# Kernel optimization log

Measured on AMD Instinct MI355X. Metric: run time of the kernel, lower is better.

The kernel has to match this reference:

```python
import jax, jax.numpy as jnp
import numpy as np

B, P = 4, 2048
NUM_MODS, D_TIME = 22, 8
DIM_S = NUM_MODS + D_TIME + 1          # 31
PHI_W, PSI_W, PSI_LAT = 32, 32, 32
DOT, HEADS, RHO_W = 16, 4, 64


def _xavier(key, shape):
    fan_in, fan_out = shape[0], shape[1]
    std = (2.0 / (fan_in + fan_out)) ** 0.5
    return jax.random.normal(key, shape, jnp.float32) * std


def setup_inputs() -> dict:
    key = jax.random.key(0)
    ks = jax.random.split(key, 20)
    inp = {
        "times": jnp.sort(jax.random.uniform(ks[0], (B, P), jnp.float32) * 100.0, axis=1),
        "values": jax.random.normal(ks[1], (B, P), jnp.float32),
        "measurements": jax.random.randint(ks[2], (B, P), 0, NUM_MODS + 1, jnp.int64 if jax.config.jax_enable_x64 else jnp.int32),
        "non_pad_mask": jnp.ones((B, P, 1), jnp.float32),
        # attention.psi MLP_state(dim_s -> psi_width)
        "psi_w1": _xavier(ks[3], (DIM_S, PSI_W)), "psi_b1": jnp.zeros((PSI_W,), jnp.float32),
        "psi_w2": _xavier(ks[4], (PSI_W, PSI_W)), "psi_b2": jnp.zeros((PSI_W,), jnp.float32),
        # attention.rho Linear(psi_width -> psi_latent_width)
        "arho_w": _xavier(ks[5], (PSI_W, PSI_LAT)), "arho_b": jnp.zeros((PSI_LAT,), jnp.float32),
        # attention key/query projections
        "W_k": _xavier(ks[6], (PSI_LAT + DIM_S, DOT * HEADS)),
        "W_q": _xavier(ks[7], (HEADS, DOT)),
        # phi MLP_state(dim_s -> phi_width)
        "phi_w1": _xavier(ks[8], (DIM_S, PHI_W)), "phi_b1": jnp.zeros((PHI_W,), jnp.float32),
        "phi_w2": _xavier(ks[9], (PHI_W, PHI_W)), "phi_b2": jnp.zeros((PHI_W,), jnp.float32),
        # rho MLP_state(n_heads*phi_width -> rho_width)
        "rho_w1": _xavier(ks[10], (HEADS * PHI_W, RHO_W)), "rho_b1": jnp.zeros((RHO_W,), jnp.float32),
        "rho_w2": _xavier(ks[11], (RHO_W, RHO_W)), "rho_b2": jnp.zeros((RHO_W,), jnp.float32),
    }
    return inp


def _mlp_state(x, mask, w1, b1, w2, b2):
    # MLP_state: relu(fc1(x*mask)); relu(fc2(h*mask)); h*mask  (dropout p=0)
    h = jax.nn.relu((x * mask) @ w1 + b1)
    h = jax.nn.relu((h * mask) @ w2 + b2)
    return h * mask


def _forward(times, values, measurements, non_pad_mask,
             psi_w1, psi_b1, psi_w2, psi_b2, arho_w, arho_b, W_k, W_q,
             phi_w1, phi_b1, phi_w2, phi_b2, rho_w1, rho_b1, rho_w2, rho_b2):
    mask = non_pad_mask  # [B,P,1]
    # temporal encoding: time / 10000^(2*(i//2)/d_time), sin on even, cos on odd
    idx = jnp.arange(D_TIME)
    pos_vec = jnp.power(10000.0, 2.0 * (idx // 2).astype(jnp.float32) / D_TIME)
    r = times[:, :, None] / pos_vec[None, None, :]          # [B,P,d_time]
    tenc = jnp.where(idx % 2 == 0, jnp.sin(r), jnp.cos(r))
    # one-hot measurements, drop padding channel 0
    meas = jax.nn.one_hot(measurements, NUM_MODS + 1, dtype=jnp.float32)[:, :, 1:]
    combined = jnp.concatenate([tenc, values[:, :, None], meas], axis=-1)  # [B,P,dim_s]

    # --- CumulativeSetAttentionLayer ---
    enc_psi = _mlp_state(combined, mask, psi_w1, psi_b1, psi_w2, psi_b2)   # [B,P,psi_w]
    counts = jnp.arange(1, P + 1, dtype=jnp.float32)[None, :, None]
    agg = jnp.cumsum(enc_psi, axis=1) / counts * mask                      # cumulative mean
    agg = (agg @ arho_w + arho_b) * mask                                   # [B,P,psi_lat]
    comb2 = jnp.concatenate([combined, agg], axis=-1)                      # [B,P,dim_s+psi_lat]
    keys = (comb2 @ W_k) * mask                                            # [B,P,DOT*HEADS]
    # torch.split(keys, n_heads, -1) + stack(-1): chunk i has size HEADS -> [B,P,HEADS,DOT]
    keys = keys.reshape(B, P, DOT, HEADS).transpose(0, 1, 3, 2)            # [B,P,h,d]
    preattn = jnp.einsum('bphd,hd->bph', keys, W_q) / jnp.sqrt(jnp.float32(DOT))
    preattn = preattn * mask                                               # [B,P,m]

    # --- phi encoding ---
    enc = _mlp_state(combined, mask, phi_w1, phi_b1, phi_w2, phi_b2)       # [B,P,d_phi]

    # --- cumulative causal softmax weighting ---
    A = preattn[:, None, :, :]                                             # [B,1,Q,m]
    Bc = jax.lax.cummax(preattn, axis=1)[:, :, None, :]                    # [B,P,1,m]
    triu = jnp.triu(jnp.ones((P, P), bool), 1)[None, :, :, None]           # mask Q > P
    D = jnp.exp(jnp.where(triu, -jnp.inf, A - Bc))                          # [B,P,Q,m]
    E = jnp.sum(D, axis=2)                                                 # [B,P,m]
    out5 = jnp.einsum('bpqm,bqd->bpmd', D, enc) / E[:, :, :, None]
    out5 = out5 * mask[:, :, :, None]                                      # [B,P,m,d_phi]

    agg2 = out5.reshape(B, P, HEADS * PHI_W)
    output = _mlp_state(agg2, mask, rho_w1, rho_b1, rho_w2, rho_b2)        # [B,P,rho_w]
    return output


def reference(times, values, measurements, non_pad_mask,
              psi_w1, psi_b1, psi_w2, psi_b2, arho_w, arho_b, W_k, W_q,
              phi_w1, phi_b1, phi_w2, phi_b2, rho_w1, rho_b1, rho_w2, rho_b2):
    return _forward(times, values, measurements, non_pad_mask,
                    psi_w1, psi_b1, psi_w2, psi_b2, arho_w, arho_b, W_k, W_q,
                    phi_w1, phi_b1, phi_w2, phi_b2, rho_w1, rho_b1, rho_w2, rho_b2)
```

## Files before the change

kernel.cpp:

```cpp
#include <hip/hip_runtime.h>
#include <math.h>

#define PB 2048
#define OFF_ENC 0
#define OFF_Q   262144
#define OFF_R   294912
#define OFF_MSK 327680
#define OFF_WV  335872

__global__ __launch_bounds__(64) void k_encode(
    const float* __restrict__ times, const float* __restrict__ vals,
    const int* __restrict__ meas, const float* __restrict__ mask,
    const float* __restrict__ psi_w1, const float* __restrict__ psi_b1,
    const float* __restrict__ psi_w2, const float* __restrict__ psi_b2,
    const float* __restrict__ phi_w1, const float* __restrict__ phi_b1,
    const float* __restrict__ phi_w2, const float* __restrict__ phi_b2,
    const float* __restrict__ arho_w, const float* __restrict__ arho_b,
    const float* __restrict__ W_k, const float* __restrict__ W_q,
    float* __restrict__ ws)
{
    __shared__ float sW[4222];
    __shared__ float sU[31*4];
    __shared__ float sU2[32*4];
    __shared__ float sV[32*4];
    __shared__ float sCc[4];
    for (int i = threadIdx.x; i < 1023; i += 64) {
        int r = i / 33, cc = i - r * 33;
        sW[i]        = (cc < 32) ? psi_w1[r*32 + cc] : 0.0f;
        sW[2111 + i] = (cc < 32) ? phi_w1[r*32 + cc] : 0.0f;
    }
    for (int i = threadIdx.x; i < 1024; i += 64) {
        sW[1055 + i] = psi_w2[i];
        sW[3166 + i] = phi_w2[i];
    }
    if (threadIdx.x < 32) {
        int i = threadIdx.x;
        sW[1023 + i] = psi_b1[i];
        sW[2079 + i] = psi_b2[i];
        sW[3134 + i] = phi_b1[i];
        sW[4190 + i] = phi_b2[i];
    }
    for (int t = threadIdx.x; t < 252; t += 64) {
        int i = t >> 2, h = t & 3;
        float s = 0.0f;
        #pragma unroll
        for (int d = 0; d < 16; d++)
            s = fmaf(W_k[i*64 + d*4 + h], W_q[h*16 + d], s);
        s *= 0.25f;
        if (i < 31) sU[i*4 + h] = s; else sU2[(i-31)*4 + h] = s;
    }
    __syncthreads();
    for (int t = threadIdx.x; t < 128; t += 64) {
        int ch = t >> 2, h = t & 3;
        float s = 0.0f;
        #pragma unroll
        for (int j = 0; j < 32; j++)
            s = fmaf(arho_w[ch*32 + j], sU2[j*4 + h], s);
        sV[t] = s;
    }
    if (threadIdx.x < 4) {
        float s = 0.0f;
        #pragma unroll
        for (int j = 0; j < 32; j++)
            s = fmaf(arho_b[j], sU2[j*4 + threadIdx.x], s);
        sCc[threadIdx.x] = s;
    }
    __syncthreads();

    const int tid  = threadIdx.x;
    const int qd   = tid >> 4;
    const int jb   = qd << 3;
    const int pp = blockIdx.x * 16 + (tid & 15);
    const int b = pp >> 11, p = pp & 2047;
    const float t = times[pp];
    const float v = vals[pp];
    const float msk = mask[pp];
    const int m = meas[pp];

    float c[9];
    c[0] = sinf(t);           c[1] = cosf(t);
    c[2] = sinf(t * 0.1f);    c[3] = cosf(t * 0.1f);
    c[4] = sinf(t * 0.01f);   c[5] = cosf(t * 0.01f);
    c[6] = sinf(t * 0.001f);  c[7] = cosf(t * 0.001f);
    c[8] = v;

    float* enc_t = ws + OFF_ENC;
    const int cb = b * 32;

    float x[9];
    #pragma unroll
    for (int i = 0; i < 9; i++) x[i] = c[i] * msk;
    const float ohs = (m > 0) ? msk : 0.0f;
    const int   ohr = (m > 0) ? (8 + m) * 33 : 0;

    if (qd == 0) {
        float r[4] = {sCc[0], sCc[1], sCc[2], sCc[3]};
        #pragma unroll
        for (int i = 0; i < 9; i++) {
            #pragma unroll
            for (int h = 0; h < 4; h++) r[h] = fmaf(c[i], sU[i*4 + h], r[h]);
        }
        if (m > 0) {
            #pragma unroll
            for (int h = 0; h < 4; h++) r[h] += sU[(8 + m)*4 + h];
        }
        #pragma unroll
        for (int h = 0; h < 4; h++)
            ws[OFF_R + (size_t)(b*4 + h) * PB + p] = r[h];
        ws[OFF_MSK + (size_t)b * PB + p] = msk;
    }

    const bool hi1 = (qd & 1) != 0;
    const bool hi2 = (qd >> 1) != 0;

    {
        float h1o[8];
        #pragma unroll
        for (int jj = 0; jj < 8; jj++) {
            const int j = jb + jj;
            float acc = sW[1023 + j];
            #pragma unroll
            for (int i = 0; i < 9; i++) acc = fmaf(x[i], sW[i*33 + j], acc);
            acc = fmaf(ohs, sW[ohr + j], acc);
            h1o[jj] = fmaxf(acc, 0.0f) * msk;
        }
        float hA[16];
        #pragma unroll
        for (int jj = 0; jj < 8; jj++) {
            const float other = __shfl_xor(h1o[jj], 16);
            hA[jj]     = hi1 ? other   : h1o[jj];
            hA[8 + jj] = hi1 ? h1o[jj] : other;
        }
        float h1f[32];
        #pragma unroll
        for (int jj = 0; jj < 16; jj++) {
            const float other = __shfl_xor(hA[jj], 32);
            h1f[jj]      = hi2 ? other  : hA[jj];
            h1f[16 + jj] = hi2 ? hA[jj] : other;
        }
        float q[4] = {0.f, 0.f, 0.f, 0.f};
        #pragma unroll
        for (int jj = 0; jj < 8; jj++) {
            const int j = jb + jj;
            float acc = sW[2079 + j];
            #pragma unroll
            for (int i = 0; i < 32; i++) acc = fmaf(h1f[i], sW[1055 + i*32 + j], acc);
            const float p2 = fmaxf(acc, 0.0f) * msk;
            #pragma unroll
            for (int h = 0; h < 4; h++) q[h] = fmaf(p2, sV[j*4 + h], q[h]);
        }
        #pragma unroll
        for (int h = 0; h < 4; h++) {
            q[h] += __shfl_xor(q[h], 16);
            q[h] += __shfl_xor(q[h], 32);
        }
        if (qd == 0) {
            #pragma unroll
            for (int h = 0; h < 4; h++)
                ws[OFF_Q + (size_t)(b*4 + h) * PB + p] = q[h];
        }
    }
    {
        float h1o[8];
        #pragma unroll
        for (int jj = 0; jj < 8; jj++) {
            const int j = jb + jj;
            float acc = sW[3134 + j];
            #pragma unroll
            for (int i = 0; i < 9; i++) acc = fmaf(x[i], sW[2111 + i*33 + j], acc);
            acc = fmaf(ohs, sW[2111 + ohr + j], acc);
            h1o[jj] = fmaxf(acc, 0.0f) * msk;
        }
        float hA[16];
        #pragma unroll
        for (int jj = 0; jj < 8; jj++) {
            const float other = __shfl_xor(h1o[jj], 16);
            hA[jj]     = hi1 ? other   : h1o[jj];
            hA[8 + jj] = hi1 ? h1o[jj] : other;
        }
        float h1f[32];
        #pragma unroll
        for (int jj = 0; jj < 16; jj++) {
            const float other = __shfl_xor(hA[jj], 32);
            h1f[jj]      = hi2 ? other  : hA[jj];
            h1f[16 + jj] = hi2 ? hA[jj] : other;
        }
        #pragma unroll
        for (int jj = 0; jj < 8; jj++) {
            const int j = jb + jj;
            float acc = sW[4190 + j];
            #pragma unroll
            for (int i = 0; i < 32; i++) acc = fmaf(h1f[i], sW[3166 + i*32 + j], acc);
            enc_t[(size_t)(cb + j) * PB + p] = fmaxf(acc, 0.0f) * msk;
        }
    }
}

__global__ __launch_bounds__(64) void k_mid(float* __restrict__ ws)
{
    const int blk = blockIdx.x;
    const int bh = blk / 33;
    const int c  = blk - bh * 33;
    const int b  = bh >> 2;
    const int lane = threadIdx.x;

    const float4* q4 = (const float4*)(ws + OFF_Q   + (size_t)bh * PB + lane * 32);
    const float4* r4 = (const float4*)(ws + OFF_R   + (size_t)bh * PB + lane * 32);
    const float4* m4 = (const float4*)(ws + OFF_MSK + (size_t)b  * PB + lane * 32);
    const float4* e4 = (const float4*)(ws + OFF_ENC + ((size_t)(b*32 + (c-1))) * PB + lane * 32);
    float4* o4 = (float4*)(ws + OFF_WV + ((size_t)(bh*33 + c)) * PB + lane * 32);

    float vq[32];
    #pragma unroll
    for (int k = 0; k < 8; k++) {
        float4 f = q4[k];
        vq[4*k] = f.x; vq[4*k+1] = f.y; vq[4*k+2] = f.z; vq[4*k+3] = f.w;
    }
    #pragma unroll
    for (int j = 1; j < 32; j++) vq[j] += vq[j-1];
    {
        const float tot = vq[31];
        float x = tot;
        #pragma unroll
        for (int off = 1; off < 64; off <<= 1) {
            float y = __shfl_up(x, off);
            if (lane >= off) x += y;
        }
        const float excl = x - tot;
        #pragma unroll
        for (int j = 0; j < 32; j++) vq[j] += excl;
    }
    float v[32];
    #pragma unroll
    for (int k = 0; k < 8; k++) {
        const float4 fr = r4[k];
        const float4 fm = m4[k];
        const int p0 = lane * 32 + 4*k;
        v[4*k+0] = expf(fm.x * (fr.x + vq[4*k+0] / (float)(p0 + 1)));
        v[4*k+1] = expf(fm.y * (fr.y + vq[4*k+1] / (float)(p0 + 2)));
        v[4*k+2] = expf(fm.z * (fr.z + vq[4*k+2] / (float)(p0 + 3)));
        v[4*k+3] = expf(fm.w * (fr.w + vq[4*k+3] / (float)(p0 + 4)));
    }
    if (c > 0) {
        #pragma unroll
        for (int k = 0; k < 8; k++) {
            float4 f = e4[k];
            v[4*k] *= f.x; v[4*k+1] *= f.y; v[4*k+2] *= f.z; v[4*k+3] *= f.w;
        }
    }
    #pragma unroll
    for (int j = 1; j < 32; j++) v[j] += v[j-1];
    const float tot = v[31];
    float x = tot;
    #pragma unroll
    for (int off = 1; off < 64; off <<= 1) {
        float y = __shfl_up(x, off);
        if (lane >= off) x += y;
    }
    const float excl = x - tot;
    #pragma unroll
    for (int j = 0; j < 32; j++) v[j] += excl;
    #pragma unroll
    for (int k = 0; k < 8; k++)
        o4[k] = make_float4(v[4*k], v[4*k+1], v[4*k+2], v[4*k+3]);
}

__global__ __launch_bounds__(256) void k_rho(
    const float* __restrict__ rho_w1, const float* __restrict__ rho_b1,
    const float* __restrict__ rho_w2, const float* __restrict__ rho_b2,
    const float* __restrict__ ws, float* __restrict__ out)
{
    __shared__ float h1s[16][65];
    __shared__ float scl[16][4];
    __shared__ float mskS[16];
    const int tid = threadIdx.x;
    const int pos = tid >> 4;
    const int g   = tid & 15;
    const int pbase = blockIdx.x * 16;
    const int b  = pbase >> 11;
    const int p0 = pbase & 2047;
    const float* wv = ws + OFF_WV + (size_t)b * 132 * PB;

    if (tid < 64) {
        const int pp = tid >> 2, h = tid & 3;
        const float msk = ws[OFF_MSK + (size_t)b * PB + p0 + pp];
        const float L = wv[(size_t)(h*33) * PB + p0 + pp];
        scl[pp][h] = msk / L;
        if (h == 0) mskS[pp] = msk;
    }
    __syncthreads();

    const int pg = p0 + pos;
    float4 acc = ((const float4*)rho_b1)[g];
    const float4* w14 = (const float4*)rho_w1;
    const float sc0 = scl[pos][0], sc1 = scl[pos][1];
    const float sc2 = scl[pos][2], sc3 = scl[pos][3];
    #pragma unroll
    for (int h = 0; h < 4; h++) {
        const float sc = (h == 0) ? sc0 : (h == 1) ? sc1 : (h == 2) ? sc2 : sc3;
        const float* wvh = wv + (size_t)(h*33 + 1) * PB + pg;
        #pragma unroll 8
        for (int d = 0; d < 32; d++) {
            const float ai = wvh[(size_t)d * PB] * sc;
            const float4 w = w14[(h*32 + d)*16 + g];
            acc.x = fmaf(ai, w.x, acc.x);
            acc.y = fmaf(ai, w.y, acc.y);
            acc.z = fmaf(ai, w.z, acc.z);
            acc.w = fmaf(ai, w.w, acc.w);
        }
    }
    const float msk = mskS[pos];
    h1s[pos][g*4+0] = fmaxf(acc.x, 0.f) * msk;
    h1s[pos][g*4+1] = fmaxf(acc.y, 0.f) * msk;
    h1s[pos][g*4+2] = fmaxf(acc.z, 0.f) * msk;
    h1s[pos][g*4+3] = fmaxf(acc.w, 0.f) * msk;
    __syncthreads();

    float4 acc2 = ((const float4*)rho_b2)[g];
    const float4* w24 = (const float4*)rho_w2;
    #pragma unroll 16
    for (int i = 0; i < 64; i++) {
        const float hv = h1s[pos][i];
        const float4 w = w24[i*16 + g];
        acc2.x = fmaf(hv, w.x, acc2.x);
        acc2.y = fmaf(hv, w.y, acc2.y);
        acc2.z = fmaf(hv, w.z, acc2.z);
        acc2.w = fmaf(hv, w.w, acc2.w);
    }
    float4 o;
    o.x = fmaxf(acc2.x, 0.f) * msk;
    o.y = fmaxf(acc2.y, 0.f) * msk;
    o.z = fmaxf(acc2.z, 0.f) * msk;
    o.w = fmaxf(acc2.w, 0.f) * msk;
    ((float4*)out)[(size_t)(pbase + pos) * 16 + g] = o;
}

extern "C" void kernel_launch(void* const* d_in, const int* in_sizes, int n_in,
                              void* d_out, int out_size, void* d_ws, size_t ws_size,
                              hipStream_t stream)
{
    const float* times  = (const float*)d_in[0];
    const float* vals   = (const float*)d_in[1];
    const int*   meas   = (const int*)d_in[2];
    const float* mask   = (const float*)d_in[3];
    const float* psi_w1 = (const float*)d_in[4];
    const float* psi_b1 = (const float*)d_in[5];
    const float* psi_w2 = (const float*)d_in[6];
    const float* psi_b2 = (const float*)d_in[7];
    const float* arho_w = (const float*)d_in[8];
    const float* arho_b = (const float*)d_in[9];
    const float* W_k    = (const float*)d_in[10];
    const float* W_q    = (const float*)d_in[11];
    const float* phi_w1 = (const float*)d_in[12];
    const float* phi_b1 = (const float*)d_in[13];
    const float* phi_w2 = (const float*)d_in[14];
    const float* phi_b2 = (const float*)d_in[15];
    const float* rho_w1 = (const float*)d_in[16];
    const float* rho_b1 = (const float*)d_in[17];
    const float* rho_w2 = (const float*)d_in[18];
    const float* rho_b2 = (const float*)d_in[19];
    float* ws  = (float*)d_ws;
    float* out = (float*)d_out;

    k_encode<<<dim3(512), dim3(64), 0, stream>>>(times, vals, meas, mask,
        psi_w1, psi_b1, psi_w2, psi_b2, phi_w1, phi_b1, phi_w2, phi_b2,
        arho_w, arho_b, W_k, W_q, ws);
    k_mid<<<dim3(528), dim3(64), 0, stream>>>(ws);
    k_rho<<<dim3(512), dim3(256), 0, stream>>>(rho_w1, rho_b1, rho_w2, rho_b2, ws, out);
}
```

Measured before the change: 132.6 us.

## Split encode MLP output columns across 8 lanes with float4 LDS weight reads

```diff
diff --git a/kernel.cpp b/kernel.cpp
--- a/kernel.cpp
+++ b/kernel.cpp
@@ -8,7 +8,17 @@
 #define OFF_MSK 327680
 #define OFF_WV  335872
 
-__global__ __launch_bounds__(64) void k_encode(
+#define S_PSI_W1 0
+#define S_PSI_B1 1116
+#define S_PSI_W2 1148
+#define S_PSI_B2 2172
+#define S_PHI_W1 2204
+#define S_PHI_B1 3320
+#define S_PHI_W2 3352
+#define S_PHI_B2 4376
+#define S_TOT    4408
+
+__global__ __launch_bounds__(128) void k_encode(
     const float* __restrict__ times, const float* __restrict__ vals,
     const int* __restrict__ meas, const float* __restrict__ mask,
     const float* __restrict__ psi_w1, const float* __restrict__ psi_b1,
@@ -19,58 +29,84 @@
     const float* __restrict__ W_k, const float* __restrict__ W_q,
     float* __restrict__ ws)
 {
-    __shared__ float sW[4222];
-    __shared__ float sU[31*4];
-    __shared__ float sU2[32*4];
-    __shared__ float sV[32*4];
-    __shared__ float sCc[4];
-    for (int i = threadIdx.x; i < 1023; i += 64) {
-        int r = i / 33, cc = i - r * 33;
-        sW[i]        = (cc < 32) ? psi_w1[r*32 + cc] : 0.0f;
-        sW[2111 + i] = (cc < 32) ? phi_w1[r*32 + cc] : 0.0f;
-    }
-    for (int i = threadIdx.x; i < 1024; i += 64) {
-        sW[1055 + i] = psi_w2[i];
-        sW[3166 + i] = phi_w2[i];
-    }
-    if (threadIdx.x < 32) {
-        int i = threadIdx.x;
-        sW[1023 + i] = psi_b1[i];
-        sW[2079 + i] = psi_b2[i];
-        sW[3134 + i] = phi_b1[i];
-        sW[4190 + i] = phi_b2[i];
-    }
-    for (int t = threadIdx.x; t < 252; t += 64) {
-        int i = t >> 2, h = t & 3;
-        float s = 0.0f;
-        #pragma unroll
-        for (int d = 0; d < 16; d++)
-            s = fmaf(W_k[i*64 + d*4 + h], W_q[h*16 + d], s);
-        s *= 0.25f;
-        if (i < 31) sU[i*4 + h] = s; else sU2[(i-31)*4 + h] = s;
+    __shared__ __align__(16) float sW[S_TOT];
+    __shared__ __align__(16) float sU[31*4];
+    __shared__ __align__(16) float sU2[32*4];
+    __shared__ __align__(16) float sV[32*4];
+    __shared__ __align__(16) float sCc[4];
+
+    const int tid = threadIdx.x;
+
+    {
+        const float4* a4 = (const float4*)psi_w1;
+        const float4* b4 = (const float4*)phi_w1;
+        float4* d1 = (float4*)&sW[S_PSI_W1];
+        float4* d2 = (float4*)&sW[S_PHI_W1];
+        for (int i = tid; i < 248; i += 128) {
+            const int r = i >> 3, c4 = i & 7;
+            d1[r*9 + c4] = a4[i];
+            d2[r*9 + c4] = b4[i];
+        }
+    }
+    {
+        const float4* p4 = (const float4*)psi_w2;
+        const float4* f4 = (const float4*)phi_w2;
+        float4* s1 = (float4*)&sW[S_PSI_W2];
+        float4* s2 = (float4*)&sW[S_PHI_W2];
+        for (int i = tid; i < 256; i += 128) { s1[i] = p4[i]; s2[i] = f4[i]; }
+    }
+    if (tid < 32) {
+        sW[S_PSI_B1 + tid] = psi_b1[tid];
+        sW[S_PSI_B2 + tid] = psi_b2[tid];
+        sW[S_PHI_B1 + tid] = phi_b1[tid];
+        sW[S_PHI_B2 + tid] = phi_b2[tid];
+    }
+    if (tid < 63) {
+        const int i = tid;
+        const float4* wk4 = (const float4*)(W_k + i*64);
+        float4 s = make_float4(0.f, 0.f, 0.f, 0.f);
+        #pragma unroll
+        for (int d = 0; d < 16; d++) {
+            const float4 w = wk4[d];
+            s.x = fmaf(w.x, W_q[d],      s.x);
+            s.y = fmaf(w.y, W_q[16 + d], s.y);
+            s.z = fmaf(w.z, W_q[32 + d], s.z);
+            s.w = fmaf(w.w, W_q[48 + d], s.w);
+        }
+        s.x *= 0.25f; s.y *= 0.25f; s.z *= 0.25f; s.w *= 0.25f;
+        if (i < 31) *(float4*)&sU[i*4]        = s;
+        else        *(float4*)&sU2[(i-31)*4]  = s;
     }
     __syncthreads();
-    for (int t = threadIdx.x; t < 128; t += 64) {
-        int ch = t >> 2, h = t & 3;
-        float s = 0.0f;
-        #pragma unroll
-        for (int j = 0; j < 32; j++)
-            s = fmaf(arho_w[ch*32 + j], sU2[j*4 + h], s);
-        sV[t] = s;
-    }
-    if (threadIdx.x < 4) {
-        float s = 0.0f;
-        #pragma unroll
-        for (int j = 0; j < 32; j++)
-            s = fmaf(arho_b[j], sU2[j*4 + threadIdx.x], s);
-        sCc[threadIdx.x] = s;
+    if (tid < 32) {
+        const float* aw = arho_w + tid*32;
+        float4 s = make_float4(0.f, 0.f, 0.f, 0.f);
+        #pragma unroll
+        for (int j = 0; j < 32; j++) {
+            const float a = aw[j];
+            const float4 u = *(const float4*)&sU2[j*4];
+            s.x = fmaf(a, u.x, s.x); s.y = fmaf(a, u.y, s.y);
+            s.z = fmaf(a, u.z, s.z); s.w = fmaf(a, u.w, s.w);
+        }
+        *(float4*)&sV[tid*4] = s;
+    } else if (tid == 32) {
+        float4 s = make_float4(0.f, 0.f, 0.f, 0.f);
+        #pragma unroll
+        for (int j = 0; j < 32; j++) {
+            const float a = arho_b[j];
+            const float4 u = *(const float4*)&sU2[j*4];
+            s.x = fmaf(a, u.x, s.x); s.y = fmaf(a, u.y, s.y);
+            s.z = fmaf(a, u.z, s.z); s.w = fmaf(a, u.w, s.w);
+        }
+        *(float4*)&sCc[0] = s;
     }
     __syncthreads();
 
-    const int tid  = threadIdx.x;
-    const int qd   = tid >> 4;
-    const int jb   = qd << 3;
-    const int pp = blockIdx.x * 16 + (tid & 15);
+    const int wv_  = tid >> 6;
+    const int lane = tid & 63;
+    const int qd   = lane >> 3;
+    const int jb   = qd << 2;
+    const int pp = blockIdx.x * 16 + wv_ * 8 + (lane & 7);
     const int b = pp >> 11, p = pp & 2047;
     const float t = times[pp];
     const float v = vals[pp];
@@ -91,66 +127,94 @@
     #pragma unroll
     for (int i = 0; i < 9; i++) x[i] = c[i] * msk;
     const float ohs = (m > 0) ? msk : 0.0f;
-    const int   ohr = (m > 0) ? (8 + m) * 33 : 0;
+    const int   ohr = (m > 0) ? (8 + m) * 36 : 0;
 
     if (qd == 0) {
-        float r[4] = {sCc[0], sCc[1], sCc[2], sCc[3]};
+        float4 r = *(const float4*)&sCc[0];
         #pragma unroll
         for (int i = 0; i < 9; i++) {
-            #pragma unroll
-            for (int h = 0; h < 4; h++) r[h] = fmaf(c[i], sU[i*4 + h], r[h]);
+            const float4 u = *(const float4*)&sU[i*4];
+            const float cv = c[i];
+            r.x = fmaf(cv, u.x, r.x); r.y = fmaf(cv, u.y, r.y);
+            r.z = fmaf(cv, u.z, r.z); r.w = fmaf(cv, u.w, r.w);
         }
         if (m > 0) {
-            #pragma unroll
-            for (int h = 0; h < 4; h++) r[h] += sU[(8 + m)*4 + h];
-        }
-        #pragma unroll
-        for (int h = 0; h < 4; h++)
-            ws[OFF_R + (size_t)(b*4 + h) * PB + p] = r[h];
+            const float4 u = *(const float4*)&sU[(8 + m)*4];
+            r.x += u.x; r.y += u.y; r.z += u.z; r.w += u.w;
+        }
+        ws[OFF_R + (size_t)(b*4 + 0) * PB + p] = r.x;
+        ws[OFF_R + (size_t)(b*4 + 1) * PB + p] = r.y;
+        ws[OFF_R + (size_t)(b*4 + 2) * PB + p] = r.z;
+        ws[OFF_R + (size_t)(b*4 + 3) * PB + p] = r.w;
         ws[OFF_MSK + (size_t)b * PB + p] = msk;
     }
 
-    const bool hi1 = (qd & 1) != 0;
-    const bool hi2 = (qd >> 1) != 0;
+    const bool hiA = (qd & 1) != 0;
+    const bool hiB = (qd & 2) != 0;
+    const bool hiC = (qd & 4) != 0;
 
     {
-        float h1o[8];
+        float4 a1 = *(const float4*)&sW[S_PSI_B1 + jb];
+        #pragma unroll
+        for (int i = 0; i < 9; i++) {
+            const float4 w = *(const float4*)&sW[S_PSI_W1 + i*36 + jb];
+            const float xv = x[i];
+            a1.x = fmaf(xv, w.x, a1.x); a1.y = fmaf(xv, w.y, a1.y);
+            a1.z = fmaf(xv, w.z, a1.z); a1.w = fmaf(xv, w.w, a1.w);
+        }
+        {
+            const float4 w = *(const float4*)&sW[S_PSI_W1 + ohr + jb];
+            a1.x = fmaf(ohs, w.x, a1.x); a1.y = fmaf(ohs, w.y, a1.y);
+            a1.z = fmaf(ohs, w.z, a1.z); a1.w = fmaf(ohs, w.w, a1.w);
+        }
+        float h1o[4];
+        h1o[0] = fmaxf(a1.x, 0.f) * msk; h1o[1] = fmaxf(a1.y, 0.f) * msk;
+        h1o[2] = fmaxf(a1.z, 0.f) * msk; h1o[3] = fmaxf(a1.w, 0.f) * msk;
+
+        float hA[8];
+        #pragma unroll
+        for (int jj = 0; jj < 4; jj++) {
+            const float other = __shfl_xor(h1o[jj], 8);
+            hA[jj]     = hiA ? other   : h1o[jj];
+            hA[4 + jj] = hiA ? h1o[jj] : other;
+        }
+        float hB[16];
         #pragma unroll
         for (int jj = 0; jj < 8; jj++) {
-            const int j = jb + jj;
-            float acc = sW[1023 + j];
-            #pragma unroll
-            for (int i = 0; i < 9; i++) acc = fmaf(x[i], sW[i*33 + j], acc);
-            acc = fmaf(ohs, sW[ohr + j], acc);
-            h1o[jj] = fmaxf(acc, 0.0f) * msk;
-        }
-        float hA[16];
-        #pragma unroll
-        for (int jj = 0; jj < 8; jj++) {
-            const float other = __shfl_xor(h1o[jj], 16);
-            hA[jj]     = hi1 ? other   : h1o[jj];
-            hA[8 + jj] = hi1 ? h1o[jj] : other;
+            const float other = __shfl_xor(hA[jj], 16);
+            hB[jj]     = hiB ? other  : hA[jj];
+            hB[8 + jj] = hiB ? hA[jj] : other;
         }
         float h1f[32];
         #pragma unroll
         for (int jj = 0; jj < 16; jj++) {
-            const float other = __shfl_xor(hA[jj], 32);
-            h1f[jj]      = hi2 ? other  : hA[jj];
-            h1f[16 + jj] = hi2 ? hA[jj] : other;
-        }
+            const float other = __shfl_xor(hB[jj], 32);
+            h1f[jj]      = hiC ? other  : hB[jj];
+            h1f[16 + jj] = hiC ? hB[jj] : other;
+        }
+        float4 a2 = *(const float4*)&sW[S_PSI_B2 + jb];
+        #pragma unroll
+        for (int i = 0; i < 32; i++) {
+            const float4 w = *(const float4*)&sW[S_PSI_W2 + i*32 + jb];
+            const float hv = h1f[i];
+            a2.x = fmaf(hv, w.x, a2.x); a2.y = fmaf(hv, w.y, a2.y);
+            a2.z = fmaf(hv, w.z, a2.z); a2.w = fmaf(hv, w.w, a2.w);
+        }
+        float p2[4];
+        p2[0] = fmaxf(a2.x, 0.f) * msk; p2[1] = fmaxf(a2.y, 0.f) * msk;
+        p2[2] = fmaxf(a2.z, 0.f) * msk; p2[3] = fmaxf(a2.w, 0.f) * msk;
         float q[4] = {0.f, 0.f, 0.f, 0.f};
         #pragma unroll
-        for (int jj = 0; jj < 8; jj++) {
-            const int j = jb + jj;
-            float acc = sW[2079 + j];
-            #pragma unroll
-            for (int i = 0; i < 32; i++) acc = fmaf(h1f[i], sW[1055 + i*32 + j], acc);
-            const float p2 = fmaxf(acc, 0.0f) * msk;
-            #pragma unroll
-            for (int h = 0; h < 4; h++) q[h] = fmaf(p2, sV[j*4 + h], q[h]);
+        for (int jj = 0; jj < 4; jj++) {
+            const float4 vv = *(const float4*)&sV[(jb + jj)*4];
+            q[0] = fmaf(p2[jj], vv.x, q[0]);
+            q[1] = fmaf(p2[jj], vv.y, q[1]);
+            q[2] = fmaf(p2[jj], vv.z, q[2]);
+            q[3] = fmaf(p2[jj], vv.w, q[3]);
         }
         #pragma unroll
         for (int h = 0; h < 4; h++) {
+            q[h] += __shfl_xor(q[h], 8);
             q[h] += __shfl_xor(q[h], 16);
             q[h] += __shfl_xor(q[h], 32);
         }
@@ -161,38 +225,56 @@
         }
     }
     {
-        float h1o[8];
+        float4 a1 = *(const float4*)&sW[S_PHI_B1 + jb];
+        #pragma unroll
+        for (int i = 0; i < 9; i++) {
+            const float4 w = *(const float4*)&sW[S_PHI_W1 + i*36 + jb];
+            const float xv = x[i];
+            a1.x = fmaf(xv, w.x, a1.x); a1.y = fmaf(xv, w.y, a1.y);
+            a1.z = fmaf(xv, w.z, a1.z); a1.w = fmaf(xv, w.w, a1.w);
+        }
+        {
+            const float4 w = *(const float4*)&sW[S_PHI_W1 + ohr + jb];
+            a1.x = fmaf(ohs, w.x, a1.x); a1.y = fmaf(ohs, w.y, a1.y);
+            a1.z = fmaf(ohs, w.z, a1.z); a1.w = fmaf(ohs, w.w, a1.w);
+        }
+        float h1o[4];
+        h1o[0] = fmaxf(a1.x, 0.f) * msk; h1o[1] = fmaxf(a1.y, 0.f) * msk;
+        h1o[2] = fmaxf(a1.z, 0.f) * msk; h1o[3] = fmaxf(a1.w, 0.f) * msk;
+
+        float hA[8];
+        #pragma unroll
+        for (int jj = 0; jj < 4; jj++) {
+            const float other = __shfl_xor(h1o[jj], 8);
+            hA[jj]     = hiA ? other   : h1o[jj];
+            hA[4 + jj] = hiA ? h1o[jj] : other;
+        }
+        float hB[16];
         #pragma unroll
         for (int jj = 0; jj < 8; jj++) {
-            const int j = jb + jj;
-            float acc = sW[3134 + j];
-            #pragma unroll
-            for (int i = 0; i < 9; i++) acc = fmaf(x[i], sW[2111 + i*33 + j], acc);
-            acc = fmaf(ohs, sW[2111 + ohr + j], acc);
-            h1o[jj] = fmaxf(acc, 0.0f) * msk;
-        }
-        float hA[16];
-        #pragma unroll
-        for (int jj = 0; jj < 8; jj++) {
-            const float other = __shfl_xor(h1o[jj], 16);
-            hA[jj]     = hi1 ? other   : h1o[jj];
-            hA[8 + jj] = hi1 ? h1o[jj] : other;
+            const float other = __shfl_xor(hA[jj], 16);
+            hB[jj]     = hiB ? other  : hA[jj];
+            hB[8 + jj] = hiB ? hA[jj] : other;
         }
         float h1f[32];
         #pragma unroll
         for (int jj = 0; jj < 16; jj++) {
-            const float other = __shfl_xor(hA[jj], 32);
-            h1f[jj]      = hi2 ? other  : hA[jj];
-            h1f[16 + jj] = hi2 ? hA[jj] : other;
-        }
-        #pragma unroll
-        for (int jj = 0; jj < 8; jj++) {
-            const int j = jb + jj;
-            float acc = sW[4190 + j];
-            #pragma unroll
-            for (int i = 0; i < 32; i++) acc = fmaf(h1f[i], sW[3166 + i*32 + j], acc);
-            enc_t[(size_t)(cb + j) * PB + p] = fmaxf(acc, 0.0f) * msk;
-        }
+            const float other = __shfl_xor(hB[jj], 32);
+            h1f[jj]      = hiC ? other  : hB[jj];
+            h1f[16 + jj] = hiC ? hB[jj] : other;
+        }
+        float4 a2 = *(const float4*)&sW[S_PHI_B2 + jb];
+        #pragma unroll
+        for (int i = 0; i < 32; i++) {
+            const float4 w = *(const float4*)&sW[S_PHI_W2 + i*32 + jb];
+            const float hv = h1f[i];
+            a2.x = fmaf(hv, w.x, a2.x); a2.y = fmaf(hv, w.y, a2.y);
+            a2.z = fmaf(hv, w.z, a2.z); a2.w = fmaf(hv, w.w, a2.w);
+        }
+        enc_t[(size_t)(cb + jb + 0) * PB + p] = fmaxf(a2.x, 0.f) * msk;
+        enc_t[(size_t)(cb + jb + 1) * PB + p] = fmaxf(a2.y, 0.f) * msk;
+        enc_t[(size_t)(cb + jb + 2) * PB + p] = fmaxf(a2.z, 0.f) * msk;
+        enc_t[(size_t)(cb + jb + 3) * PB + p] = fmaxf(a2.w, 0.f) * msk;
     }
 }
 
@@ -362,7 +444,7 @@
     float* ws  = (float*)d_ws;
     float* out = (float*)d_out;
 
-    k_encode<<<dim3(512), dim3(64), 0, stream>>>(times, vals, meas, mask,
+    k_encode<<<dim3(512), dim3(128), 0, stream>>>(times, vals, meas, mask,
         psi_w1, psi_b1, psi_w2, psi_b2, phi_w1, phi_b1, phi_w2, phi_b2,
         arho_w, arho_b, W_k, W_q, ws);
     k_mid<<<dim3(528), dim3(64), 0, stream>>>(ws);
```

Result: faster. 128.3 us (-3.2%).
